# Kernel optimization log

Measured on AMD Instinct MI355X. Metric: run time of the kernel, lower is better.

## Reference

```python
import jax, jax.numpy as jnp
import numpy as np

C = 320        # in_channels == inner_dim (n_heads*d_head = 8*40)
HEADS = 8
DH = 40
CTX = 768
FF_INNER = 1280  # 4*C
G = 32         # GroupNorm groups


def _ln(x, w, b, eps=1e-5):
    m = x.mean(-1, keepdims=True)
    v = ((x - m) ** 2).mean(-1, keepdims=True)
    return (x - m) * jax.lax.rsqrt(v + eps) * w + b


def _attn(q, k, v, heads, scale):
    # faithful to source: split last dim as (d h) -> head index is fastest
    B, Lq, D = q.shape
    Lk = k.shape[1]
    dh = D // heads
    q = q.reshape(B, Lq, dh, heads).transpose(0, 3, 1, 2)  # b h i d
    k = k.reshape(B, Lk, dh, heads).transpose(0, 3, 1, 2)  # b h j d
    v = v.reshape(B, Lk, dh, heads).transpose(0, 3, 1, 2)
    sim = jnp.einsum('bhid,bhjd->bhij', q, k) * scale
    w = jax.nn.softmax(sim, axis=-1)
    o = jnp.einsum('bhij,bhjd->bhid', w, v)
    # merge as (h d): head index is slowest on output (matches source)
    return o.transpose(0, 2, 1, 3).reshape(B, Lq, heads * dh)


def setup_inputs() -> dict:
    key = jax.random.key(0)
    ks = jax.random.split(key, 20)
    n = lambda i, shape: jax.random.normal(ks[i], shape, jnp.float32) * 0.02
    z = lambda d: jnp.zeros((d,), jnp.float32)
    o = lambda d: jnp.ones((d,), jnp.float32)
    return dict(
        x=jax.random.normal(ks[0], (1, C, 64, 64), jnp.float32),
        context=jax.random.normal(ks[1], (1, 77, CTX), jnp.float32),
        gn_w=o(C), gn_b=z(C),
        w_in=n(2, (C, C)), b_in=z(C),
        ln1_w=o(C), ln1_b=z(C),
        wq1=n(3, (C, C)), wk1=n(4, (C, C)), wv1=n(5, (C, C)),
        wo1=n(6, (C, C)), bo1=z(C),
        ln2_w=o(C), ln2_b=z(C),
        wq2=n(7, (C, C)), wk2=n(8, (CTX, C)), wv2=n(9, (CTX, C)),
        wo2=n(10, (C, C)), bo2=z(C),
        ln3_w=o(C), ln3_b=z(C),
        wff1=n(11, (C, 2 * FF_INNER)), bff1=z(2 * FF_INNER),
        wff2=n(12, (FF_INNER, C)), bff2=z(C),
        w_out=n(13, (C, C)), b_out=z(C),
    )


def reference(x, context, gn_w, gn_b, w_in, b_in,
              ln1_w, ln1_b, wq1, wk1, wv1, wo1, bo1,
              ln2_w, ln2_b, wq2, wk2, wv2, wo2, bo2,
              ln3_w, ln3_b, wff1, bff1, wff2, bff2,
              w_out, b_out):
    B, Cc, H, W = x.shape
    scale = DH ** (-0.5)
    x_in = x
    # GroupNorm(32, eps=1e-6)
    g = x.reshape(B, G, Cc // G, H, W)
    m = g.mean((2, 3, 4), keepdims=True)
    v = ((g - m) ** 2).mean((2, 3, 4), keepdims=True)
    h = ((g - m) * jax.lax.rsqrt(v + 1e-6)).reshape(B, Cc, H, W)
    h = h * gn_w[None, :, None, None] + gn_b[None, :, None, None]
    # 1x1 conv in_proj
    h = jnp.einsum('bchw,co->bohw', h, w_in) + b_in[None, :, None, None]
    # b c h w -> b (h w) c
    t = h.transpose(0, 2, 3, 1).reshape(B, H * W, C)
    # --- transformer block (depth=1) ---
    # attn_1: self-attn; NOTE source applies k/v proj to the QUERY projection
    hn = _ln(t, ln1_w, ln1_b)
    q = hn @ wq1
    k = q @ wk1
    vv = q @ wv1
    t = t + (_attn(q, k, vv, HEADS, scale) @ wo1 + bo1)
    # attn_2: cross-attn with context
    hn = _ln(t, ln2_w, ln2_b)
    q = hn @ wq2
    k = context @ wk2
    vv = context @ wv2
    t = t + (_attn(q, k, vv, HEADS, scale) @ wo2 + bo2)
    # GEGLU feed-forward
    hn = _ln(t, ln3_w, ln3_b)
    p = hn @ wff1 + bff1
    a, gate = p[..., :FF_INNER], p[..., FF_INNER:]
    t = t + ((a * jax.nn.gelu(gate, approximate=False)) @ wff2 + bff2)
    # b (h w) c -> b c h w
    s = t.reshape(B, H, W, C).transpose(0, 3, 1, 2)
    out = jnp.einsum('bchw,co->bohw', s, w_out) + b_out[None, :, None, None]
    return out + x_in
```

## Files before the change

kernel.cpp:

```cpp
#include <hip/hip_runtime.h>
#include <hip/hip_bf16.h>
#include <math.h>

#define CCH 320
#define NHEADS 8
#define DH 40
#define HW 4096
#define FFI 1280

typedef __bf16 bf16x8 __attribute__((ext_vector_type(8)));
typedef unsigned short u16x8 __attribute__((ext_vector_type(8)));
typedef short s16x4 __attribute__((ext_vector_type(4)));
typedef float f32x4 __attribute__((ext_vector_type(4)));
typedef unsigned int u32x4 __attribute__((ext_vector_type(4)));

__device__ inline unsigned short f2bf(float f) {
    __hip_bfloat16 h = __float2bfloat16(f);
    return __builtin_bit_cast(unsigned short, h);
}
__device__ inline unsigned pk2bf(float a, float b) {
#if __has_builtin(__builtin_amdgcn_cvt_pk_bf16_f32)
    typedef __bf16 bf16x2 __attribute__((ext_vector_type(2)));
    bf16x2 r = __builtin_amdgcn_cvt_pk_bf16_f32(a, b);
    return __builtin_bit_cast(unsigned, r);
#else
    return (unsigned)f2bf(a) | ((unsigned)f2bf(b) << 16);
#endif
}
__device__ inline float bf2f(unsigned short u) {
    return __builtin_bit_cast(float, ((unsigned)u) << 16);
}
__device__ inline bf16x8 ldfrag(const unsigned short* p) {
    u16x8 raw = *reinterpret_cast<const u16x8*>(p);
    return __builtin_bit_cast(bf16x8, raw);
}
__device__ inline s16x4 pk2frag(unsigned a, unsigned b) {
    unsigned long long v = (unsigned long long)a | ((unsigned long long)b << 32);
    return __builtin_bit_cast(s16x4, v);
}

__device__ inline float ex2(float x) {
#if __has_builtin(__builtin_amdgcn_exp2f)
    return __builtin_amdgcn_exp2f(x);
#else
    return exp2f(x);
#endif
}
__device__ inline float fast_rcp(float x) {
#if __has_builtin(__builtin_amdgcn_rcpf)
    return __builtin_amdgcn_rcpf(x);
#else
    return 1.f / x;
#endif
}
__device__ inline float fast_gelu(float x) {
    float z = fabsf(x) * 0.70710678118654752f;
    float t = fast_rcp(fmaf(0.3275911f, z, 1.f));
    float poly = fmaf(fmaf(fmaf(fmaf(1.061405429f, t, -1.453152027f), t,
                               1.421413741f), t, -0.284496736f), t,
                      0.254829592f) * t;
    float e = ex2(z * z * -1.4426950408889634f);
    float erfz = 1.f - poly * e;
    float s = copysignf(erfz, x);
    return 0.5f * x * (1.f + s);
}

__global__ __launch_bounds__(256) void prep_w2(
    const float* __restrict__ w_in, const float* __restrict__ wq1,
    const float* __restrict__ wk1, const float* __restrict__ wv1,
    const float* __restrict__ wo1, const float* __restrict__ wq2,
    const float* __restrict__ wo2, const float* __restrict__ w_out,
    const float* __restrict__ wff1, const float* __restrict__ wff2,
    const float* __restrict__ wk2, const float* __restrict__ wv2,
    unsigned short* __restrict__ Wt) {
    __shared__ float tile[64][65];
    const int b = blockIdx.x, tid = threadIdx.x;
    const float* src;
    int K, stride, dstoff, k0, n0;
    bool glu = false;
    if (b < 200) {
        int m = b / 25, t = b % 25;
        k0 = (t / 5) * 64; n0 = (t % 5) * 64;
        K = 320; stride = 320; dstoff = m * 102400;
        src = (m == 0) ? w_in : (m == 1) ? wq1 : (m == 2) ? wk1 :
              (m == 3) ? wv1 : (m == 4) ? wo1 : (m == 5) ? wq2 :
              (m == 6) ? wo2 : w_out;
    } else if (b < 300) {
        int t = b - 200;
        k0 = (t / 5) * 64; n0 = (t % 5) * 64;
        K = 1280; stride = 320; dstoff = 1638400; src = wff2;
    } else if (b < 500) {
        int t = b - 300;
        k0 = (t / 40) * 64; n0 = (t % 40) * 64;
        K = 320; stride = 2560; dstoff = 819200; src = wff1; glu = true;
    } else if (b < 560) {
        int t = b - 500;
        k0 = (t / 5) * 64; n0 = (t % 5) * 64;
        K = 768; stride = 320; dstoff = 2048000; src = wk2;
    } else {
        int t = b - 560;
        k0 = (t / 5) * 64; n0 = (t % 5) * 64;
        K = 768; stride = 320; dstoff = 2048000 + 245760; src = wv2;
    }
#pragma unroll
    for (int i = 0; i < 16; ++i) {
        int idx = tid + i * 256;
        int r = idx >> 6, cn = idx & 63;
        int scol = glu ? ((n0 >> 1) + (cn >> 1) + (cn & 1) * FFI) : (n0 + cn);
        tile[r][cn] = src[(size_t)(k0 + r) * stride + scol];
    }
    __syncthreads();
#pragma unroll
    for (int i = 0; i < 16; ++i) {
        int idx = tid + i * 256;
        int cl = idx >> 6, cr = idx & 63;
        Wt[dstoff + (size_t)(n0 + cl) * K + k0 + cr] = f2bf(tile[cr][cl]);
    }
}

__global__ void pack_ctx(const float* __restrict__ ctx,
                         unsigned short* __restrict__ D) {
    int idx = blockIdx.x * 256 + threadIdx.x;
    int row = idx / 768, col = idx - row * 768;
    float v = (row < 77) ? ctx[row * 768 + col] : 0.f;
    D[idx] = f2bf(v);
}

__global__ __launch_bounds__(256) void gn_stats(const float* __restrict__ X,
                                                float2* __restrict__ part) {
    __shared__ float s1[256], s2[256];
    const int b = blockIdx.x, tid = threadIdx.x;
    const float* xg = X + b * 5120;
    float s = 0.f, sq = 0.f;
#pragma unroll
    for (int i = 0; i < 20; ++i) { float v = xg[tid + i * 256]; s += v; sq += v * v; }
    s1[tid] = s; s2[tid] = sq; __syncthreads();
    for (int off = 128; off > 0; off >>= 1) {
        if (tid < off) { s1[tid] += s1[tid + off]; s2[tid] += s2[tid + off]; }
        __syncthreads();
    }
    if (tid == 0) part[b] = make_float2(s1[0], s2[0]);
}

__global__ __launch_bounds__(256) void gn_apply(const float* __restrict__ X,
                                                const float2* __restrict__ part,
                                                const float* __restrict__ w,
                                                const float* __restrict__ b,
                                                unsigned short* __restrict__ Y) {
    __shared__ float tile[64][65];
    __shared__ float gm[32], gr[32];
    const int tid = threadIdx.x;
    const int hw0 = blockIdx.x * 64, c0 = blockIdx.y * 64;
    if (tid < 32) {
        float s = 0.f, sq = 0.f;
#pragma unroll
        for (int i = 0; i < 8; ++i) { float2 p = part[tid * 8 + i]; s += p.x; sq += p.y; }
        float mean = s * (1.f / 40960.f);
        float var  = sq * (1.f / 40960.f) - mean * mean;
        gm[tid] = mean; gr[tid] = rsqrtf(var + 1e-6f);
    }
#pragma unroll
    for (int i = 0; i < 16; ++i) {
        int idx = tid + i * 256;
        int r = idx >> 6, col = idx & 63;
        tile[r][col] = X[(size_t)(c0 + r) * HW + hw0 + col];
    }
    __syncthreads();
#pragma unroll
    for (int i = 0; i < 16; ++i) {
        int idx = tid + i * 256;
        int hwl = idx >> 6, cl = idx & 63;
        int c = c0 + cl, g = c / 10;
        float v = (tile[cl][hwl] - gm[g]) * gr[g] * w[c] + b[c];
        Y[(size_t)(hw0 + hwl) * CCH + c] = f2bf(v);
    }
}

__global__ __launch_bounds__(256) void ln_kernel(const float* __restrict__ X,
                                                 const float* __restrict__ w,
                                                 const float* __restrict__ b,
                                                 unsigned short* __restrict__ Y) {
    const int row  = blockIdx.x * 4 + (threadIdx.x >> 6);
    const int lane = threadIdx.x & 63;
    const float* xr = X + row * CCH;
    const float4 a = *(const float4*)(xr + lane * 4);
    const float  e = xr[256 + lane];
    float v[5] = {a.x, a.y, a.z, a.w, e};
    float s = 0.f, sq = 0.f;
#pragma unroll
    for (int i = 0; i < 5; ++i) { s += v[i]; sq += v[i] * v[i]; }
#pragma unroll
    for (int off = 32; off > 0; off >>= 1) {
        s  += __shfl_xor(s, off, 64);
        sq += __shfl_xor(sq, off, 64);
    }
    const float mean = s * (1.f / 320.f);
    const float var  = sq * (1.f / 320.f) - mean * mean;
    const float rstd = rsqrtf(var + 1e-5f);
    unsigned short* yr = Y + row * CCH;
    const float4 w4 = *(const float4*)(w + lane * 4);
    const float4 b4 = *(const float4*)(b + lane * 4);
    float r0 = (v[0] - mean) * rstd * w4.x + b4.x;
    float r1 = (v[1] - mean) * rstd * w4.y + b4.y;
    float r2 = (v[2] - mean) * rstd * w4.z + b4.z;
    float r3 = (v[3] - mean) * rstd * w4.w + b4.w;
    *(uint2*)(yr + lane * 4) = make_uint2(pk2bf(r0, r1), pk2bf(r2, r3));
    int ct = 256 + lane;
    yr[ct] = f2bf((v[4] - mean) * rstd * w[ct] + b[ct]);
}

template <int MT, int K>
__global__ __launch_bounds__(256) void gemm4(
    const unsigned short* __restrict__ A,
    const unsigned short* __restrict__ Bt,
    const float* __restrict__ bias,
    const float* __restrict__ res,
    void* __restrict__ Cout, void* __restrict__ Cout2,
    int N, int mode, float scale) {
    constexpr int NCH = K / 64;
    __shared__ __align__(16) unsigned short Ab[2][MT * 16 * 64];
    __shared__ __align__(16) unsigned short Bb[2][64 * 64];
    const int tid  = threadIdx.x;
    const int wave = tid >> 6, lane = tid & 63;
    const int quad = lane >> 4, c = lane & 15;
    const int m0 = blockIdx.y * (MT * 16);
    const int bn = blockIdx.x;

    f32x4 acc[MT];
#pragma unroll
    for (int i = 0; i < MT; ++i) acc[i] = (f32x4){0.f, 0.f, 0.f, 0.f};

    const unsigned short* aslab = A + (size_t)m0 * K;
    const unsigned short* bslab = Bt + (size_t)(bn * 64) * K;

    constexpr int ITA = MT * 16 * 8 / 256;
    int arow[ITA], aoff[ITA];
#pragma unroll
    for (int i = 0; i < ITA; ++i) {
        int idx = tid + i * 256;
        arow[i] = idx >> 3;
        int g = idx & 7;
        aoff[i] = arow[i] * 64 + ((g ^ (arow[i] & 7)) * 8);
    }
    int brow[2], boff[2];
#pragma unroll
    for (int i = 0; i < 2; ++i) {
        int idx = tid + i * 256;
        brow[i] = idx >> 3;
        int g = idx & 7;
        boff[i] = brow[i] * 64 + ((g ^ (brow[i] & 7)) * 8);
    }
    const int ag = (tid & 7) * 8;

    {
        u16x8 ra[ITA], rb[2];
#pragma unroll
        for (int i = 0; i < ITA; ++i)
            ra[i] = *(const u16x8*)(aslab + (size_t)arow[i] * K + ag);
#pragma unroll
        for (int i = 0; i < 2; ++i)
            rb[i] = *(const u16x8*)(bslab + (size_t)brow[i] * K + ag);
#pragma unroll
        for (int i = 0; i < ITA; ++i) *(u16x8*)&Ab[0][aoff[i]] = ra[i];
#pragma unroll
        for (int i = 0; i < 2; ++i) *(u16x8*)&Bb[0][boff[i]] = rb[i];
    }
    __syncthreads();

    const int swz0 = (quad ^ (c & 7)) * 8;
    const int swz1 = ((quad + 4) ^ (c & 7)) * 8;
#pragma unroll
    for (int ch = 0; ch < NCH; ++ch) {
        const int buf = ch & 1;
        u16x8 ra[ITA], rb[2];
        if (ch + 1 < NCH) {
            const int kb = (ch + 1) * 64;
#pragma unroll
            for (int i = 0; i < ITA; ++i)
                ra[i] = *(const u16x8*)(aslab + (size_t)arow[i] * K + kb + ag);
#pragma unroll
            for (int i = 0; i < 2; ++i)
                rb[i] = *(const u16x8*)(bslab + (size_t)brow[i] * K + kb + ag);
        }
        bf16x8 b0 = ldfrag(&Bb[buf][(wave * 16 + c) * 64 + swz0]);
        bf16x8 b1 = ldfrag(&Bb[buf][(wave * 16 + c) * 64 + swz1]);
#pragma unroll
        for (int mt = 0; mt < MT; ++mt) {
            bf16x8 a0 = ldfrag(&Ab[buf][(mt * 16 + c) * 64 + swz0]);
            bf16x8 a1 = ldfrag(&Ab[buf][(mt * 16 + c) * 64 + swz1]);
            acc[mt] = __builtin_amdgcn_mfma_f32_16x16x32_bf16(a0, b0, acc[mt], 0, 0, 0);
            acc[mt] = __builtin_amdgcn_mfma_f32_16x16x32_bf16(a1, b1, acc[mt], 0, 0, 0);
        }
        if (ch + 1 < NCH) {
            const int nb = buf ^ 1;
#pragma unroll
            for (int i = 0; i < ITA; ++i) *(u16x8*)&Ab[nb][aoff[i]] = ra[i];
#pragma unroll
            for (int i = 0; i < 2; ++i) *(u16x8*)&Bb[nb][boff[i]] = rb[i];
        }
        __syncthreads();
    }

    const int col = bn * 64 + wave * 16 + c;
    float bval = 0.f;
    if (bias) bval = (mode == 5) ? bias[(col >> 1) + (col & 1) * FFI] : bias[col];

    if (mode == 9) {
#pragma unroll
        for (int mt = 0; mt < MT; ++mt) {
            const int row0 = m0 + mt * 16 + quad * 4;
            float4 xv = *(const float4*)(res + (size_t)col * HW + row0);
            float4 ov;
            ov.x = acc[mt][0] + bval + xv.x;
            ov.y = acc[mt][1] + bval + xv.y;
            ov.z = acc[mt][2] + bval + xv.z;
            ov.w = acc[mt][3] + bval + xv.w;
            *(float4*)((float*)Cout + (size_t)col * HW + row0) = ov;
        }
        return;
    }
#pragma unroll
    for (int mt = 0; mt < MT; ++mt) {
#pragma unroll
        for (int r = 0; r < 4; ++r) {
            const int row = m0 + mt * 16 + quad * 4 + r;
            float v = acc[mt][r];
            if (mode == 0) {
                v += bval;
                if (res) v += res[(size_t)row * N + col];
                ((float*)Cout)[(size_t)row * N + col] = v;
            } else if (mode == 2) {
                int h = col & 7, d = col >> 3;
                ((unsigned short*)Cout)[(((size_t)h << 12) + row) * 64 + d] = f2bf(v * scale);
                if (d < 24)
                    ((unsigned short*)Cout)[(((size_t)h << 12) + row) * 64 + 40 + d] = 0;
            } else if (mode == 4) {
                ((unsigned short*)Cout)[(size_t)row * N + col] =
                    f2bf(v + bval + res[(size_t)row * N + col]);
            } else if (mode == 5) {
                v += bval;
                float other = __shfl_xor(v, 1, 64);
                if ((c & 1) == 0) {
                    float g = fast_gelu(other);
                    ((unsigned short*)Cout)[(size_t)row * FFI + (col >> 1)] = f2bf(v * g);
                }
            } else if (mode == 6) {
                ((unsigned short*)Cout)[(size_t)row * N + col] = f2bf(v);
                int h = col & 7, d = col >> 3;
                ((unsigned short*)Cout2)[(((size_t)h << 12) + row) * 64 + d] = f2bf(v * scale);
                if (d < 24)
                    ((unsigned short*)Cout2)[(((size_t)h << 12) + row) * 64 + 40 + d] = 0;
            } else if (mode == 7) {
                if (col < 320) {
                    int h = col & 7, d = col >> 3;
                    ((unsigned short*)Cout)[(((size_t)h << 12) + row) * 64 + d] = f2bf(v);
                    if (d < 24)
                        ((unsigned short*)Cout)[(((size_t)h << 12) + row) * 64 + 40 + d] = 0;
                } else {
                    int c2 = col - 320;
                    int h = c2 & 7, d = c2 >> 3;
                    ((unsigned short*)Cout2)[(((size_t)(h * 48 + d)) << 12) + row] = f2bf(v);
                    if (d < 8)
                        ((unsigned short*)Cout2)[(((size_t)(h * 48 + 40 + d)) << 12) + row] =
                            (d == 0) ? (unsigned short)0x3F80 : (unsigned short)0;
                }
            } else {
                if (col < 320) {
                    int h = col & 7, d = col >> 3;
                    ((unsigned short*)Cout)[(((size_t)h << 7) + row) * 64 + d] = f2bf(v);
                    if (d < 24)
                        ((unsigned short*)Cout)[(((size_t)h << 7) + row) * 64 + 40 + d] = 0;
                } else {
                    int c2 = col - 320;
                    int h = c2 & 7, d = c2 >> 3;
                    ((unsigned short*)Cout2)[(size_t)(h * 48 + d) * 128 + row] = f2bf(v);
                    if (d < 8)
                        ((unsigned short*)Cout2)[(size_t)(h * 48 + 40 + d) * 128 + row] =
                            (d == 0) ? (unsigned short)0x3F80 : (unsigned short)0;
                }
            }
        }
    }
}

template <int TILES, bool MASK, bool FINAL>
__global__ __launch_bounds__(256) void attn8(
    const unsigned short* __restrict__ Qp,
    const unsigned short* __restrict__ Kp,
    const unsigned short* __restrict__ Vt,
    float* __restrict__ pO, float* __restrict__ pL,
    unsigned short* __restrict__ Ofin,
    int Lk, int Lkp) {
    __shared__ __align__(16) unsigned short Kb[2][64 * 64];
    __shared__ __align__(16) unsigned short Vb[2][48 * 64];
    const int tid  = threadIdx.x;
    const int wave = tid >> 6, lane = tid & 63;
    const int quad = lane >> 4, c = lane & 15;
    const int id  = blockIdx.x;
    const int h   = id & 7;
    const int qt  = (id >> 3) & 31;
    const int seg = id >> 8;
    const int q0  = qt * 128 + wave * 32;

    const unsigned short* qbaseA = Qp + ((((size_t)h << 12) + q0 + c) << 6) + quad * 8;
    const bf16x8 bQA0 = ldfrag(qbaseA);
    const bf16x8 bQA1 = ldfrag(qbaseA + 32);
    const bf16x8 bQB0 = ldfrag(qbaseA + 1024);
    const bf16x8 bQB1 = ldfrag(qbaseA + 1024 + 32);

    f32x4 oA[3], oB[3];
#pragma unroll
    for (int i = 0; i < 3; ++i) {
        oA[i] = (f32x4){0.f, 0.f, 0.f, 0.f};
        oB[i] = (f32x4){0.f, 0.f, 0.f, 0.f};
    }

    const int kt0 = seg * TILES;
    const unsigned short* kglob = Kp + (((size_t)h * Lkp + kt0 * 64) << 6);
    const unsigned short* vglob = Vt + ((size_t)h * 48) * Lkp + kt0 * 64;

    const int r0 = lane >> 3;
    const int g  = lane & 7;
    int ldsoff[4];
    const unsigned short* gptr0[4];
#pragma unroll
    for (int i = 0; i < 4; ++i) {
        int s = wave + 4 * i;
        if (s < 8) {
            int row = s * 8 + r0;
            ldsoff[i] = row * 64 + (g ^ (row & 7)) * 8;
            gptr0[i]  = kglob + (size_t)row * 64 + g * 8;
        } else if (s < 14) {
            int d = (s - 8) * 8 + r0;
            ldsoff[i] = d * 64 + (g ^ (d & 7)) * 8;
            gptr0[i]  = vglob + (size_t)d * Lkp + g * 8;
        } else {
            ldsoff[i] = 0; gptr0[i] = nullptr;
        }
    }
    const bool isK[4] = {(wave + 0) < 8, (wave + 4) < 8, (wave + 8) < 8, (wave + 12) < 8};
    const bool act[4] = {true, true, true, (wave + 12) < 14};

    {
        u16x8 st[4];
#pragma unroll
        for (int i = 0; i < 4; ++i)
            if (act[i]) st[i] = *(const u16x8*)(gptr0[i]);
#pragma unroll
        for (int i = 0; i < 4; ++i)
            if (act[i]) {
                unsigned short* lp = isK[i] ? &Kb[0][ldsoff[i]] : &Vb[0][ldsoff[i]];
                *(u16x8*)lp = st[i];
            }
    }
    __syncthreads();

#pragma unroll
    for (int t = 0; t < TILES; ++t) {
        const int b = t & 1;
        u16x8 st[4];
        if (t + 1 < TILES) {
            const int kb = (t + 1) * 64;
#pragma unroll
            for (int i = 0; i < 4; ++i)
                if (act[i]) {
                    const unsigned short* gp =
                        isK[i] ? (gptr0[i] + (size_t)kb * 64) : (gptr0[i] + kb);
                    st[i] = *(const u16x8*)gp;
                }
        }
        const unsigned short* Kl = &Kb[b][0];
        const unsigned short* Vl = &Vb[b][0];
        const int sw0 = (quad ^ (c & 7)) * 8;
        const int sw1 = ((quad + 4) ^ (c & 7)) * 8;
        const int abs_kb = kt0 * 64 + t * 64;
#pragma unroll
        for (int blk = 0; blk < 4; ++blk) {
            const int row = (blk * 16 + c) * 64;
            bf16x8 k0 = ldfrag(Kl + row + sw0);
            bf16x8 k1 = ldfrag(Kl + row + sw1);
            f32x4 zA = {0.f, 0.f, 0.f, 0.f};
            zA = __builtin_amdgcn_mfma_f32_16x16x32_bf16(k0, bQA0, zA, 0, 0, 0);
            zA = __builtin_amdgcn_mfma_f32_16x16x32_bf16(k1, bQA1, zA, 0, 0, 0);
            f32x4 zB = {0.f, 0.f, 0.f, 0.f};
            zB = __builtin_amdgcn_mfma_f32_16x16x32_bf16(k0, bQB0, zB, 0, 0, 0);
            zB = __builtin_amdgcn_mfma_f32_16x16x32_bf16(k1, bQB1, zB, 0, 0, 0);
            if (MASK) {
#pragma unroll
                for (int r = 0; r < 4; ++r) {
                    bool inv = (abs_kb + blk * 16 + quad * 4 + r >= Lk);
                    zA[r] = inv ? -30000.f : zA[r];
                    zB[r] = inv ? -30000.f : zB[r];
                }
            }
            s16x4 PA = pk2frag(pk2bf(ex2(zA[0]), ex2(zA[1])),
                               pk2bf(ex2(zA[2]), ex2(zA[3])));
            s16x4 PB = pk2frag(pk2bf(ex2(zB[0]), ex2(zB[1])),
                               pk2bf(ex2(zB[2]), ex2(zB[3])));
#pragma unroll
            for (int db = 0; db < 3; ++db) {
                const int dim = db * 16 + c;
                const int off =
                    (((blk * 2 + (quad >> 1)) ^ (dim & 7)) * 8) + (quad & 1) * 4;
                s16x4 vf = *(const s16x4*)(Vl + dim * 64 + off);
                oA[db] = __builtin_amdgcn_mfma_f32_16x16x16bf16_1k(vf, PA, oA[db], 0, 0, 0);
                oB[db] = __builtin_amdgcn_mfma_f32_16x16x16bf16_1k(vf, PB, oB[db], 0, 0, 0);
            }
        }
        if (t + 1 < TILES) {
            const int nb = b ^ 1;
#pragma unroll
            for (int i = 0; i < 4; ++i)
                if (act[i]) {
                    unsigned short* lp = isK[i] ? &Kb[nb][ldsoff[i]] : &Vb[nb][ldsoff[i]];
                    *(u16x8*)lp = st[i];
                }
        }
        __syncthreads();
    }
    if (FINAL) {
        float lA = __shfl(oA[2][0], 32 + c, 64);
        float lB = __shfl(oB[2][0], 32 + c, 64);
        float liA = fast_rcp(lA), liB = fast_rcp(lB);
        unsigned short* oaptr = Ofin + (size_t)(q0 + c) * CCH + h * DH;
        unsigned short* obptr = Ofin + (size_t)(q0 + 16 + c) * CCH + h * DH;
        *(uint2*)(oaptr + quad * 4) =
            make_uint2(pk2bf(oA[0][0] * liA, oA[0][1] * liA),
                       pk2bf(oA[0][2] * liA, oA[0][3] * liA));
        *(uint2*)(oaptr + 16 + quad * 4) =
            make_uint2(pk2bf(oA[1][0] * liA, oA[1][1] * liA),
                       pk2bf(oA[1][2] * liA, oA[1][3] * liA));
        if (quad < 2)
            *(uint2*)(oaptr + 32 + quad * 4) =
                make_uint2(pk2bf(oA[2][0] * liA, oA[2][1] * liA),
                           pk2bf(oA[2][2] * liA, oA[2][3] * liA));
        *(uint2*)(obptr + quad * 4) =
            make_uint2(pk2bf(oB[0][0] * liB, oB[0][1] * liB),
                       pk2bf(oB[0][2] * liB, oB[0][3] * liB));
        *(uint2*)(obptr + 16 + quad * 4) =
            make_uint2(pk2bf(oB[1][0] * liB, oB[1][1] * liB),
                       pk2bf(oB[1][2] * liB, oB[1][3] * liB));
        if (quad < 2)
            *(uint2*)(obptr + 32 + quad * 4) =
                make_uint2(pk2bf(oB[2][0] * liB, oB[2][1] * liB),
                           pk2bf(oB[2][2] * liB, oB[2][3] * liB));
        return;
    }
    const size_t base = ((size_t)(seg * 8 + h)) << 12;
    float* obA = pO + (base + q0 + c) * 40;
    *(float4*)(obA + quad * 4)      = make_float4(oA[0][0], oA[0][1], oA[0][2], oA[0][3]);
    *(float4*)(obA + 16 + quad * 4) = make_float4(oA[1][0], oA[1][1], oA[1][2], oA[1][3]);
    if (quad < 2)
        *(float4*)(obA + 32 + quad * 4) = make_float4(oA[2][0], oA[2][1], oA[2][2], oA[2][3]);
    float* obB = pO + (base + q0 + 16 + c) * 40;
    *(float4*)(obB + quad * 4)      = make_float4(oB[0][0], oB[0][1], oB[0][2], oB[0][3]);
    *(float4*)(obB + 16 + quad * 4) = make_float4(oB[1][0], oB[1][1], oB[1][2], oB[1][3]);
    if (quad < 2)
        *(float4*)(obB + 32 + quad * 4) = make_float4(oB[2][0], oB[2][1], oB[2][2], oB[2][3]);
    if (quad == 2) {
        pL[base + q0 + c]      = oA[2][0];
        pL[base + q0 + 16 + c] = oB[2][0];
    }
}

__global__ __launch_bounds__(256) void attn_combine2(
    const float* __restrict__ pO, const float* __restrict__ pL,
    unsigned short* __restrict__ O, int S) {
    int idx = blockIdx.x * 256 + threadIdx.x;
    int h = idx / (HW * 10);
    int rem = idx - h * (HW * 10);
    int row = rem / 10, dg = rem - row * 10;
    float4 num = make_float4(0.f, 0.f, 0.f, 0.f);
    float den = 0.f;
    for (int s = 0; s < S; ++s) {
        size_t base = ((size_t)(s * 8 + h)) << 12;
        float4 p = *(const float4*)(pO + (base + row) * 40 + dg * 4);
        num.x += p.x; num.y += p.y; num.z += p.z; num.w += p.w;
        den += pL[base + row];
    }
    float inv = fast_rcp(den);
    unsigned short* ob = O + (size_t)row * CCH + h * DH + dg * 4;
    unsigned lo = pk2bf(num.x * inv, num.y * inv);
    unsigned hi = pk2bf(num.z * inv, num.w * inv);
    *(uint2*)ob = make_uint2(lo, hi);
}

extern "C" void kernel_launch(void* const* d_in, const int* in_sizes, int n_in,
                              void* d_out, int out_size, void* d_ws, size_t ws_size,
                              hipStream_t stream) {
    const float* x     = (const float*)d_in[0];
    const float* ctx   = (const float*)d_in[1];
    const float* gn_w  = (const float*)d_in[2];
    const float* gn_b  = (const float*)d_in[3];
    const float* w_in  = (const float*)d_in[4];
    const float* b_in  = (const float*)d_in[5];
    const float* ln1_w = (const float*)d_in[6];
    const float* ln1_b = (const float*)d_in[7];
    const float* wq1   = (const float*)d_in[8];
    const float* wk1   = (const float*)d_in[9];
    const float* wv1   = (const float*)d_in[10];
    const float* wo1   = (const float*)d_in[11];
    const float* bo1   = (const float*)d_in[12];
    const float* ln2_w = (const float*)d_in[13];
    const float* ln2_b = (const float*)d_in[14];
    const float* wq2   = (const float*)d_in[15];
    const float* wk2   = (const float*)d_in[16];
    const float* wv2   = (const float*)d_in[17];
    const float* wo2   = (const float*)d_in[18];
    const float* bo2   = (const float*)d_in[19];
    const float* ln3_w = (const float*)d_in[20];
    const float* ln3_b = (const float*)d_in[21];
    const float* wff1  = (const float*)d_in[22];
    const float* bff1  = (const float*)d_in[23];
    const float* wff2  = (const float*)d_in[24];
    const float* bff2  = (const float*)d_in[25];
    const float* w_out = (const float*)d_in[26];
    const float* b_out = (const float*)d_in[27];
    float* out = (float*)d_out;

    const int NT = HW * CCH;
    const size_t need8 = (size_t)4 * NT * 9 + 8 * 131072 + 2048 + 38010880;
    const int SEGS = (ws_size >= need8) ? 8 : 4;

    float* ws = (float*)d_ws;
    float* t_   = ws;
    float* pO   = t_ + NT;
    float* pL   = pO + (size_t)SEGS * NT;
    float2* gnp = (float2*)(pL + (size_t)SEGS * 8 * 4096);
    unsigned short* u = (unsigned short*)(gnp + 256);
    unsigned short* a_bf = u;                  u += NT;
    unsigned short* q_bf = u;                  u += NT;
    unsigned short* o_bf = u;                  u += NT;
    unsigned short* t_bf = u;                  u += NT;
    unsigned short* g_bf = u;                  u += HW * FFI;
    unsigned short* Qp   = u;                  u += 8 * 4096 * 64;
    unsigned short* Kp   = u;                  u += 8 * 4096 * 64;
    unsigned short* Vt   = u;                  u += 8 * 48 * 4096;
    unsigned short* Kc   = u;                  u += 8 * 128 * 64;
    unsigned short* Vc   = u;                  u += 8 * 48 * 128;
    unsigned short* Wt   = u;                  u += 2048000 + 2 * 245760;
    unsigned short* ctx_bf = u;                u += 128 * 768;

    const unsigned short* w_inT  = Wt;
    const unsigned short* wq1T   = Wt + 102400;
    const unsigned short* wk1T   = Wt + 204800;
    const unsigned short* wo1T   = Wt + 409600;
    const unsigned short* wq2T   = Wt + 512000;
    const unsigned short* wo2T   = Wt + 614400;
    const unsigned short* w_outT = Wt + 716800;
    const unsigned short* wff1T  = Wt + 819200;
    const unsigned short* wff2T  = Wt + 1638400;
    const unsigned short* wk2T   = Wt + 2048000;

    const float qscale = 0.15811388300841897f * 1.4426950408889634f;

    prep_w2<<<620, 256, 0, stream>>>(w_in, wq1, wk1, wv1, wo1, wq2, wo2, w_out,
                                     wff1, wff2, wk2, wv2, Wt);
    pack_ctx<<<384, 256, 0, stream>>>(ctx, ctx_bf);

    gn_stats<<<256, 256, 0, stream>>>(x, gnp);
    gn_apply<<<dim3(64, 5), 256, 0, stream>>>(x, gnp, gn_w, gn_b, a_bf);
    gemm4<2, 320><<<dim3(5, 128), 256, 0, stream>>>(a_bf, w_inT, b_in, nullptr, t_, nullptr, CCH, 0, 1.f);
    ln_kernel<<<1024, 256, 0, stream>>>(t_, ln1_w, ln1_b, a_bf);
    gemm4<2, 320><<<dim3(5, 128), 256, 0, stream>>>(a_bf, wq1T, nullptr, nullptr, q_bf, Qp, CCH, 6, qscale);
    gemm4<2, 320><<<dim3(10, 128), 256, 0, stream>>>(q_bf, wk1T, nullptr, nullptr, Kp, Vt, 640, 7, 1.f);
    if (SEGS == 8)
        attn8<8, false, false><<<2048, 256, 0, stream>>>(Qp, Kp, Vt, pO, pL, nullptr, HW, HW);
    else
        attn8<16, false, false><<<1024, 256, 0, stream>>>(Qp, Kp, Vt, pO, pL, nullptr, HW, HW);
    attn_combine2<<<1280, 256, 0, stream>>>(pO, pL, o_bf, SEGS);
    gemm4<2, 320><<<dim3(5, 128), 256, 0, stream>>>(o_bf, wo1T, bo1, t_, t_, nullptr, CCH, 0, 1.f);
    ln_kernel<<<1024, 256, 0, stream>>>(t_, ln2_w, ln2_b, a_bf);
    gemm4<2, 320><<<dim3(5, 128), 256, 0, stream>>>(a_bf, wq2T, nullptr, nullptr, Qp, nullptr, CCH, 2, qscale);
    gemm4<2, 768><<<dim3(10, 4), 256, 0, stream>>>(ctx_bf, wk2T, nullptr, nullptr, Kc, Vc, 640, 8, 1.f);
    attn8<2, true, true><<<256, 256, 0, stream>>>(Qp, Kc, Vc, nullptr, nullptr, o_bf, 77, 128);
    gemm4<2, 320><<<dim3(5, 128), 256, 0, stream>>>(o_bf, wo2T, bo2, t_, t_, nullptr, CCH, 0, 1.f);
    ln_kernel<<<1024, 256, 0, stream>>>(t_, ln3_w, ln3_b, a_bf);
    gemm4<2, 320><<<dim3(40, 128), 256, 0, stream>>>(a_bf, wff1T, bff1, nullptr, g_bf, nullptr, 2 * FFI, 5, 1.f);
    gemm4<2, 1280><<<dim3(5, 128), 256, 0, stream>>>(g_bf, wff2T, bff2, t_, t_bf, nullptr, CCH, 4, 1.f);
    gemm4<2, 320><<<dim3(5, 128), 256, 0, stream>>>(t_bf, w_outT, b_out, x, out, nullptr, CCH, 9, 1.f);
}
```

Measured before the change: 301.0 us.

## Precompose wq1 with wk1/wv1 and fuse prep kernels into one launch

```diff
diff --git a/kernel.cpp b/kernel.cpp
--- a/kernel.cpp
+++ b/kernel.cpp
@@ -13,6 +13,10 @@
 typedef short s16x4 __attribute__((ext_vector_type(4)));
 typedef float f32x4 __attribute__((ext_vector_type(4)));
 typedef unsigned int u32x4 __attribute__((ext_vector_type(4)));
+
+#define WQ1BF_OFF 2539520
+#define W2_OFF    2641920
+#define WT_TOTAL  2949120
 
 __device__ inline unsigned short f2bf(float f) {
     __hip_bfloat16 h = __float2bfloat16(f);
@@ -65,16 +69,51 @@
     return 0.5f * x * (1.f + s);
 }
 
-__global__ __launch_bounds__(256) void prep_w2(
+__global__ __launch_bounds__(256) void megaprep(
     const float* __restrict__ w_in, const float* __restrict__ wq1,
     const float* __restrict__ wk1, const float* __restrict__ wv1,
     const float* __restrict__ wo1, const float* __restrict__ wq2,
     const float* __restrict__ wo2, const float* __restrict__ w_out,
     const float* __restrict__ wff1, const float* __restrict__ wff2,
     const float* __restrict__ wk2, const float* __restrict__ wv2,
-    unsigned short* __restrict__ Wt) {
+    unsigned short* __restrict__ Wt,
+    const float* __restrict__ ctx, unsigned short* __restrict__ ctx_bf,
+    const float* __restrict__ X, float2* __restrict__ gnp) {
     __shared__ float tile[64][65];
+    __shared__ float s1[256], s2[256];
     const int b = blockIdx.x, tid = threadIdx.x;
+    if (b >= 670) {
+        if (b < 1054) {
+            int idx = (b - 670) * 256 + tid;
+            int row = idx / 768, col = idx - row * 768;
+            float v = (row < 77) ? ctx[row * 768 + col] : 0.f;
+            ctx_bf[idx] = f2bf(v);
+        } else {
+            const int bg = b - 1054;
+            const float* xg = X + bg * 5120;
+            float s = 0.f, sq = 0.f;
+#pragma unroll
+            for (int i = 0; i < 20; ++i) { float v = xg[tid + i * 256]; s += v; sq += v * v; }
+            s1[tid] = s; s2[tid] = sq; __syncthreads();
+            for (int off = 128; off > 0; off >>= 1) {
+                if (tid < off) { s1[tid] += s1[tid + off]; s2[tid] += s2[tid + off]; }
+                __syncthreads();
+            }
+            if (tid == 0) gnp[bg] = make_float2(s1[0], s2[0]);
+        }
+        return;
+    }
+    if (b >= 620 && b < 645) {
+        int t = b - 620;
+        int base = (t / 5) * 64 * 320 + (t % 5) * 64;
+#pragma unroll
+        for (int i = 0; i < 16; ++i) {
+            int idx = tid + i * 256;
+            int r = idx >> 6, cn = idx & 63;
+            Wt[WQ1BF_OFF + base + r * 320 + cn] = f2bf(wq1[base + r * 320 + cn]);
+        }
+        return;
+    }
     const float* src;
     int K, stride, dstoff, k0, n0;
     bool glu = false;
@@ -97,10 +136,14 @@
         int t = b - 500;
         k0 = (t / 5) * 64; n0 = (t % 5) * 64;
         K = 768; stride = 320; dstoff = 2048000; src = wk2;
-    } else {
+    } else if (b < 620) {
         int t = b - 560;
         k0 = (t / 5) * 64; n0 = (t % 5) * 64;
         K = 768; stride = 320; dstoff = 2048000 + 245760; src = wv2;
+    } else {
+        int t = b - 645;
+        k0 = (t / 5) * 64; n0 = (t % 5) * 64;
+        K = 320; stride = 320; dstoff = W2_OFF; src = wq1;
     }
 #pragma unroll
     for (int i = 0; i < 16; ++i) {
@@ -116,30 +159,6 @@
         int cl = idx >> 6, cr = idx & 63;
         Wt[dstoff + (size_t)(n0 + cl) * K + k0 + cr] = f2bf(tile[cr][cl]);
     }
-}
-
-__global__ void pack_ctx(const float* __restrict__ ctx,
-                         unsigned short* __restrict__ D) {
-    int idx = blockIdx.x * 256 + threadIdx.x;
-    int row = idx / 768, col = idx - row * 768;
-    float v = (row < 77) ? ctx[row * 768 + col] : 0.f;
-    D[idx] = f2bf(v);
-}
-
-__global__ __launch_bounds__(256) void gn_stats(const float* __restrict__ X,
-                                                float2* __restrict__ part) {
-    __shared__ float s1[256], s2[256];
-    const int b = blockIdx.x, tid = threadIdx.x;
-    const float* xg = X + b * 5120;
-    float s = 0.f, sq = 0.f;
-#pragma unroll
-    for (int i = 0; i < 20; ++i) { float v = xg[tid + i * 256]; s += v; sq += v * v; }
-    s1[tid] = s; s2[tid] = sq; __syncthreads();
-    for (int off = 128; off > 0; off >>= 1) {
-        if (tid < off) { s1[tid] += s1[tid + off]; s2[tid] += s2[tid + off]; }
-        __syncthreads();
-    }
-    if (tid == 0) part[b] = make_float2(s1[0], s2[0]);
 }
 
 __global__ __launch_bounds__(256) void gn_apply(const float* __restrict__ X,
@@ -344,27 +363,7 @@
                     float g = fast_gelu(other);
                     ((unsigned short*)Cout)[(size_t)row * FFI + (col >> 1)] = f2bf(v * g);
                 }
-            } else if (mode == 6) {
-                ((unsigned short*)Cout)[(size_t)row * N + col] = f2bf(v);
-                int h = col & 7, d = col >> 3;
-                ((unsigned short*)Cout2)[(((size_t)h << 12) + row) * 64 + d] = f2bf(v * scale);
-                if (d < 24)
-                    ((unsigned short*)Cout2)[(((size_t)h << 12) + row) * 64 + 40 + d] = 0;
-            } else if (mode == 7) {
-                if (col < 320) {
-                    int h = col & 7, d = col >> 3;
-                    ((unsigned short*)Cout)[(((size_t)h << 12) + row) * 64 + d] = f2bf(v);
-                    if (d < 24)
-                        ((unsigned short*)Cout)[(((size_t)h << 12) + row) * 64 + 40 + d] = 0;
-                } else {
-                    int c2 = col - 320;
-                    int h = c2 & 7, d = c2 >> 3;
-                    ((unsigned short*)Cout2)[(((size_t)(h * 48 + d)) << 12) + row] = f2bf(v);
-                    if (d < 8)
-                        ((unsigned short*)Cout2)[(((size_t)(h * 48 + 40 + d)) << 12) + row] =
-                            (d == 0) ? (unsigned short)0x3F80 : (unsigned short)0;
-                }
-            } else {
+            } else if (mode == 8) {
                 if (col < 320) {
                     int h = col & 7, d = col >> 3;
                     ((unsigned short*)Cout)[(((size_t)h << 7) + row) * 64 + d] = f2bf(v);
@@ -376,6 +375,29 @@
                     ((unsigned short*)Cout2)[(size_t)(h * 48 + d) * 128 + row] = f2bf(v);
                     if (d < 8)
                         ((unsigned short*)Cout2)[(size_t)(h * 48 + 40 + d) * 128 + row] =
+                            (d == 0) ? (unsigned short)0x3F80 : (unsigned short)0;
+                }
+            } else if (mode == 10) {
+                ((unsigned short*)Cout)[(size_t)col * 320 + row] = f2bf(v);
+            } else {
+                if (col < 320) {
+                    int h = col & 7, d = col >> 3;
+                    ((unsigned short*)Cout)[(((size_t)h << 12) + row) * 64 + d] = f2bf(v * scale);
+                    if (d < 24)
+                        ((unsigned short*)Cout)[(((size_t)h << 12) + row) * 64 + 40 + d] = 0;
+                } else if (col < 640) {
+                    int c2 = col - 320;
+                    int h = c2 & 7, d = c2 >> 3;
+                    ((unsigned short*)Cout2)[(((size_t)h << 12) + row) * 64 + d] = f2bf(v);
+                    if (d < 24)
+                        ((unsigned short*)Cout2)[(((size_t)h << 12) + row) * 64 + 40 + d] = 0;
+                } else {
+                    int c2 = col - 640;
+                    int h = c2 & 7, d = c2 >> 3;
+                    unsigned short* Vt_ = (unsigned short*)Cout2 + (size_t)8 * 4096 * 64;
+                    Vt_[(((size_t)(h * 48 + d)) << 12) + row] = f2bf(v);
+                    if (d < 8)
+                        Vt_[(((size_t)(h * 48 + 40 + d)) << 12) + row] =
                             (d == 0) ? (unsigned short)0x3F80 : (unsigned short)0;
                 }
             }
@@ -619,7 +641,11 @@
     float* out = (float*)d_out;
 
     const int NT = HW * CCH;
-    const size_t need8 = (size_t)4 * NT * 9 + 8 * 131072 + 2048 + 38010880;
+    const size_t u16_cnt = (size_t)NT * 3 + (size_t)HW * FFI +
+                           (size_t)8 * 4096 * 64 * 2 + (size_t)8 * 48 * 4096 +
+                           8 * 128 * 64 + 8 * 48 * 128 + WT_TOTAL + 128 * 768;
+    const size_t need8 = (size_t)4 * (NT + 8 * NT + 8 * 32768 + 512) +
+                         2 * u16_cnt + 4096;
     const int SEGS = (ws_size >= need8) ? 8 : 4;
 
     float* ws = (float*)d_ws;
@@ -629,7 +655,6 @@
     float2* gnp = (float2*)(pL + (size_t)SEGS * 8 * 4096);
     unsigned short* u = (unsigned short*)(gnp + 256);
     unsigned short* a_bf = u;                  u += NT;
-    unsigned short* q_bf = u;                  u += NT;
     unsigned short* o_bf = u;                  u += NT;
     unsigned short* t_bf = u;                  u += NT;
     unsigned short* g_bf = u;                  u += HW * FFI;
@@ -638,12 +663,10 @@
     unsigned short* Vt   = u;                  u += 8 * 48 * 4096;
     unsigned short* Kc   = u;                  u += 8 * 128 * 64;
     unsigned short* Vc   = u;                  u += 8 * 48 * 128;
-    unsigned short* Wt   = u;                  u += 2048000 + 2 * 245760;
+    unsigned short* Wt   = u;                  u += WT_TOTAL;
     unsigned short* ctx_bf = u;                u += 128 * 768;
 
     const unsigned short* w_inT  = Wt;
-    const unsigned short* wq1T   = Wt + 102400;
-    const unsigned short* wk1T   = Wt + 204800;
     const unsigned short* wo1T   = Wt + 409600;
     const unsigned short* wq2T   = Wt + 512000;
     const unsigned short* wo2T   = Wt + 614400;
@@ -651,19 +674,21 @@
     const unsigned short* wff1T  = Wt + 819200;
     const unsigned short* wff2T  = Wt + 1638400;
     const unsigned short* wk2T   = Wt + 2048000;
+    const unsigned short* wk1T   = Wt + 204800;
+    const unsigned short* Wq1bf  = Wt + WQ1BF_OFF;
+    unsigned short*       W2     = Wt + W2_OFF;
 
     const float qscale = 0.15811388300841897f * 1.4426950408889634f;
 
-    prep_w2<<<620, 256, 0, stream>>>(w_in, wq1, wk1, wv1, wo1, wq2, wo2, w_out,
-                                     wff1, wff2, wk2, wv2, Wt);
-    pack_ctx<<<384, 256, 0, stream>>>(ctx, ctx_bf);
-
-    gn_stats<<<256, 256, 0, stream>>>(x, gnp);
+    megaprep<<<1310, 256, 0, stream>>>(w_in, wq1, wk1, wv1, wo1, wq2, wo2, w_out,
+                                       wff1, wff2, wk2, wv2, Wt, ctx, ctx_bf,
+                                       x, gnp);
+    gemm4<2, 320><<<dim3(10, 10), 256, 0, stream>>>(
+        Wq1bf, wk1T, nullptr, nullptr, W2 + (size_t)320 * 320, nullptr, 640, 10, 1.f);
     gn_apply<<<dim3(64, 5), 256, 0, stream>>>(x, gnp, gn_w, gn_b, a_bf);
     gemm4<2, 320><<<dim3(5, 128), 256, 0, stream>>>(a_bf, w_inT, b_in, nullptr, t_, nullptr, CCH, 0, 1.f);
     ln_kernel<<<1024, 256, 0, stream>>>(t_, ln1_w, ln1_b, a_bf);
-    gemm4<2, 320><<<dim3(5, 128), 256, 0, stream>>>(a_bf, wq1T, nullptr, nullptr, q_bf, Qp, CCH, 6, qscale);
-    gemm4<2, 320><<<dim3(10, 128), 256, 0, stream>>>(q_bf, wk1T, nullptr, nullptr, Kp, Vt, 640, 7, 1.f);
+    gemm4<2, 320><<<dim3(15, 128), 256, 0, stream>>>(a_bf, W2, nullptr, nullptr, Qp, Kp, 960, 11, qscale);
     if (SEGS == 8)
         attn8<8, false, false><<<2048, 256, 0, stream>>>(Qp, Kp, Vt, pO, pL, nullptr, HW, HW);
     else
```

Result: faster. 294.2 us (-2.2%).
